# Kernel optimization log

Measured on AMD Instinct MI355X. Metric: run time of the kernel, lower is better.

## Reference

```python
import jax, jax.numpy as jnp
import numpy as np

D_MODEL = 1024
B, T = 4, 2048
NEG = -1000000000.0


def setup_inputs() -> dict:
    key = jax.random.key(0)
    kq, kk, kv = jax.random.split(key, 3)
    query = jax.random.normal(kq, (B, T, D_MODEL), dtype=jnp.float32)
    k = jax.random.normal(kk, (B, T, D_MODEL), dtype=jnp.float32)
    value = jax.random.normal(kv, (B, T, D_MODEL), dtype=jnp.float32)
    # causal mask: 1.0 where attention is disallowed (strictly upper triangular)
    mask = jnp.triu(jnp.ones((T, T), dtype=jnp.float32), k=1)
    return {"query": query, "key": k, "value": value, "mask": mask}


def reference(query, key, value, mask):
    # dk = sqrt(1/d_model); logits = QK^T / dk  (i.e. * sqrt(d_model)) -- faithful to source
    dk = jnp.sqrt(jnp.float32(1.0) / jnp.float32(D_MODEL))
    attn_logits = jnp.einsum("btc,bsc->bts", query, key) / dk
    attn_logits = attn_logits + mask * NEG  # mask broadcasts over batch
    score = jax.nn.softmax(attn_logits, axis=-1)
    attention = jnp.einsum("bts,bsc->btc", score, value)
    return attention
```

## Files before the change

### kernel.cpp

```cpp
#include <hip/hip_runtime.h>

#define BB 4
#define TT 2048
#define DD 1024
#define SCALE 32.0f
#define NTILE 136

typedef _Float16 f16;
typedef __attribute__((ext_vector_type(4))) _Float16 half4v;
typedef __attribute__((ext_vector_type(8))) _Float16 half8v;
typedef __attribute__((ext_vector_type(16))) float f32x16;

static __device__ inline half8v ld_frag(const f16* p) {
    half4v a = *(const half4v*)p;
    half4v b = *(const half4v*)(p + 4);
    half8v r;
    r[0] = a[0]; r[1] = a[1]; r[2] = a[2]; r[3] = a[3];
    r[4] = b[0]; r[5] = b[1]; r[6] = b[2]; r[7] = b[3];
    return r;
}

__global__ __launch_bounds__(256, 2) void k1_qk(const float* __restrict__ Q,
                                                const float* __restrict__ Kmat,
                                                float* __restrict__ S) {
    __shared__ f16 Ah[128][36], Al[128][36], Bh[128][36], Bl[128][36];

    int bid = blockIdx.x;
    int b = bid / NTILE, r = bid % NTILE;
    int mi = 0;
    while ((mi + 1) * (mi + 2) / 2 <= r) ++mi;
    int nj = r - mi * (mi + 1) / 2;

    const float* Qb = Q + ((size_t)b * TT + (size_t)mi * 128) * DD;
    const float* Kb = Kmat + ((size_t)b * TT + (size_t)nj * 128) * DD;
    float* Sb = S + (size_t)b * TT * TT + (size_t)(mi * 128) * TT + nj * 128;

    int tid = threadIdx.x;
    int lane = tid & 63;
    int wave = tid >> 6;
    int l31 = lane & 31, lhi = lane >> 5;
    int wrow = wave >> 1, wcol = wave & 1;

    int r0 = tid >> 1;
    int c0 = (tid & 1) * 16;

    f32x16 acc[2][2] = {};

    float4 abuf[4], bbuf[4];
#pragma unroll
    for (int j = 0; j < 4; ++j) {
        abuf[j] = *(const float4*)(Qb + (size_t)r0 * DD + c0 + 4 * j);
        bbuf[j] = *(const float4*)(Kb + (size_t)r0 * DD + c0 + 4 * j);
    }

    for (int ch = 0; ch < DD / 32; ++ch) {
        __syncthreads();
#pragma unroll
        for (int j = 0; j < 4; ++j) {
            float4 a = abuf[j], bq = bbuf[j];
            float ax[4] = {a.x * SCALE, a.y * SCALE, a.z * SCALE, a.w * SCALE};
            float bx[4] = {bq.x, bq.y, bq.z, bq.w};
            half4v ahv, alv, bhv, blv;
#pragma unroll
            for (int e = 0; e < 4; ++e) {
                f16 h = (f16)ax[e];
                ahv[e] = h;
                alv[e] = (f16)(ax[e] - (float)h);
                f16 g = (f16)bx[e];
                bhv[e] = g;
                blv[e] = (f16)(bx[e] - (float)g);
            }
            *(half4v*)&Ah[r0][c0 + 4 * j] = ahv;
            *(half4v*)&Al[r0][c0 + 4 * j] = alv;
            *(half4v*)&Bh[r0][c0 + 4 * j] = bhv;
            *(half4v*)&Bl[r0][c0 + 4 * j] = blv;
        }
        __syncthreads();
        if (ch + 1 < DD / 32) {
            int ck = (ch + 1) * 32;
#pragma unroll
            for (int j = 0; j < 4; ++j) {
                abuf[j] = *(const float4*)(Qb + (size_t)r0 * DD + ck + c0 + 4 * j);
                bbuf[j] = *(const float4*)(Kb + (size_t)r0 * DD + ck + c0 + 4 * j);
            }
        }
#pragma unroll
        for (int ks = 0; ks < 2; ++ks) {
            int kb = ks * 16 + lhi * 8;
            half8v ahf[2], alf[2], bhf[2], blf[2];
#pragma unroll
            for (int f = 0; f < 2; ++f) {
                ahf[f] = ld_frag(&Ah[wrow * 64 + f * 32 + l31][kb]);
                alf[f] = ld_frag(&Al[wrow * 64 + f * 32 + l31][kb]);
                bhf[f] = ld_frag(&Bh[wcol * 64 + f * 32 + l31][kb]);
                blf[f] = ld_frag(&Bl[wcol * 64 + f * 32 + l31][kb]);
            }
#pragma unroll
            for (int fm = 0; fm < 2; ++fm)
#pragma unroll
                for (int fn = 0; fn < 2; ++fn) {
                    acc[fm][fn] = __builtin_amdgcn_mfma_f32_32x32x16_f16(ahf[fm], bhf[fn], acc[fm][fn], 0, 0, 0);
                    acc[fm][fn] = __builtin_amdgcn_mfma_f32_32x32x16_f16(ahf[fm], blf[fn], acc[fm][fn], 0, 0, 0);
                    acc[fm][fn] = __builtin_amdgcn_mfma_f32_32x32x16_f16(alf[fm], bhf[fn], acc[fm][fn], 0, 0, 0);
                }
        }
    }
#pragma unroll
    for (int fm = 0; fm < 2; ++fm)
#pragma unroll
        for (int fn = 0; fn < 2; ++fn)
#pragma unroll
            for (int g = 0; g < 16; ++g) {
                int rr = (g & 3) + 8 * (g >> 2) + 4 * lhi;
                int row = wrow * 64 + fm * 32 + rr;
                int col = wcol * 64 + fn * 32 + l31;
                Sb[(size_t)row * TT + col] = acc[fm][fn][g];
            }
}

__global__ __launch_bounds__(256) void k1b_softmax(const float* __restrict__ S,
                                                   f16* __restrict__ P) {
    __shared__ float red[4];
    int rowid = blockIdx.x;
    int b = rowid >> 11, t = rowid & (TT - 1);
    const float* Sr = S + (size_t)b * TT * TT + (size_t)t * TT;
    f16* Pr = P + (size_t)b * TT * TT + (size_t)t * TT;
    int tid = threadIdx.x;
    int nv = t + 1;
    int rowend = ((t >> 7) + 1) << 7;

    float m = -3.0e38f;
    for (int c = tid; c < nv; c += 256) m = fmaxf(m, Sr[c]);
#pragma unroll
    for (int o = 32; o > 0; o >>= 1) m = fmaxf(m, __shfl_xor(m, o));
    if ((tid & 63) == 0) red[tid >> 6] = m;
    __syncthreads();
    m = fmaxf(fmaxf(red[0], red[1]), fmaxf(red[2], red[3]));
    __syncthreads();

    float s = 0.f;
    for (int c = tid; c < nv; c += 256) s += exp2f((Sr[c] - m) * 1.4426950408889634f);
#pragma unroll
    for (int o = 32; o > 0; o >>= 1) s += __shfl_xor(s, o);
    if ((tid & 63) == 0) red[tid >> 6] = s;
    __syncthreads();
    s = red[0] + red[1] + red[2] + red[3];
    float inv = 1.0f / s;

    for (int c = tid; c < rowend; c += 256) {
        float p = (c < nv) ? exp2f((Sr[c] - m) * 1.4426950408889634f) * inv : 0.0f;
        Pr[c] = (f16)p;
    }
}

__global__ __launch_bounds__(256, 2) void k2_pv(const f16* __restrict__ P,
                                                const float* __restrict__ V,
                                                float* __restrict__ O) {
    __shared__ f16 Pa[128][36];
    __shared__ f16 Vt[128][36];

    int bid = blockIdx.x;
    int b = bid >> 7;
    int rest = bid & 127;
    int mi = rest >> 3, nj = rest & 7;
    int kend = (mi + 1) * 128;

    const f16* Pb = P + (size_t)b * TT * TT + (size_t)(mi * 128) * TT;
    const float* Vb = V + (size_t)b * TT * DD + nj * 128;
    float* Ob = O + (size_t)b * TT * DD + (size_t)(mi * 128) * DD + nj * 128;

    int tid = threadIdx.x;
    int lane = tid & 63;
    int wave = tid >> 6;
    int l31 = lane & 31, lhi = lane >> 5;
    int wrow = wave >> 1, wcol = wave & 1;

    f32x16 acc[2][2] = {};

    int pr = tid >> 1, pc = (tid & 1) * 16;
    int vk = tid >> 3, vn = (tid & 7) * 16;

    uint2 pbuf[4];
    float4 vbuf[4];
#pragma unroll
    for (int j = 0; j < 4; ++j) {
        pbuf[j] = *(const uint2*)(Pb + (size_t)pr * TT + pc + 4 * j);
        vbuf[j] = *(const float4*)(Vb + (size_t)vk * DD + vn + 4 * j);
    }

    for (int ck = 0; ck < kend; ck += 32) {
        __syncthreads();
#pragma unroll
        for (int j = 0; j < 4; ++j) {
            *(uint2*)&Pa[pr][pc + 4 * j] = pbuf[j];
            float4 v = vbuf[j];
            float vv[4] = {v.x, v.y, v.z, v.w};
            int n0 = vn + 4 * j;
#pragma unroll
            for (int e = 0; e < 4; ++e) {
                int n = n0 + e;
                Vt[n][vk ^ ((((unsigned)n >> 4) & 3) << 3)] = (f16)vv[e];
            }
        }
        __syncthreads();
        if (ck + 32 < kend) {
            int cn = ck + 32;
#pragma unroll
            for (int j = 0; j < 4; ++j) {
                pbuf[j] = *(const uint2*)(Pb + (size_t)pr * TT + cn + pc + 4 * j);
                vbuf[j] = *(const float4*)(Vb + (size_t)(cn + vk) * DD + vn + 4 * j);
            }
        }
#pragma unroll
        for (int ks = 0; ks < 2; ++ks) {
            int kb = ks * 16 + lhi * 8;
            half8v paf[2], vbf[2];
#pragma unroll
            for (int f = 0; f < 2; ++f) {
                paf[f] = ld_frag(&Pa[wrow * 64 + f * 32 + l31][kb]);
                int n = wcol * 64 + f * 32 + l31;
                int kbs = kb ^ ((((unsigned)n >> 4) & 3) << 3);
                vbf[f] = ld_frag(&Vt[n][kbs]);
            }
#pragma unroll
            for (int fm = 0; fm < 2; ++fm)
#pragma unroll
                for (int fn = 0; fn < 2; ++fn)
                    acc[fm][fn] = __builtin_amdgcn_mfma_f32_32x32x16_f16(paf[fm], vbf[fn], acc[fm][fn], 0, 0, 0);
        }
    }
#pragma unroll
    for (int fm = 0; fm < 2; ++fm)
#pragma unroll
        for (int fn = 0; fn < 2; ++fn)
#pragma unroll
            for (int g = 0; g < 16; ++g) {
                int rr = (g & 3) + 8 * (g >> 2) + 4 * lhi;
                int row = wrow * 64 + fm * 32 + rr;
                int col = wcol * 64 + fn * 32 + l31;
                Ob[(size_t)row * DD + col] = acc[fm][fn][g];
            }
}

__global__ __launch_bounds__(256) void fa_fallback(const float* __restrict__ Q,
                                                   const float* __restrict__ Kmat,
                                                   const float* __restrict__ V,
                                                   float* __restrict__ O) {
    __shared__ float qs[DD];
    __shared__ float osum[DD];
    __shared__ float red[4];
    int rowid = blockIdx.x;
    int b = rowid >> 11, t = rowid & (TT - 1);
    const float* q = Q + ((size_t)b * TT + t) * DD;
    int tid = threadIdx.x;
    for (int j = tid; j < DD; j += 256) { qs[j] = q[j] * SCALE; osum[j] = 0.f; }
    __syncthreads();
    float m = -3.0e38f, l = 0.f;
    for (int s = 0; s <= t; ++s) {
        const float* kr = Kmat + ((size_t)b * TT + s) * DD;
        float part = 0.f;
#pragma unroll
        for (int j = 0; j < 4; ++j) part += qs[tid * 4 + j] * kr[tid * 4 + j];
#pragma unroll
        for (int o = 32; o > 0; o >>= 1) part += __shfl_xor(part, o);
        if ((tid & 63) == 0) red[tid >> 6] = part;
        __syncthreads();
        float dot = red[0] + red[1] + red[2] + red[3];
        float mn = fmaxf(m, dot);
        float f = exp2f((m - mn) * 1.44269504f);
        float e = exp2f((dot - mn) * 1.44269504f);
        l = l * f + e;
        const float* vr = V + ((size_t)b * TT + s) * DD;
#pragma unroll
        for (int j = 0; j < 4; ++j) {
            int c = tid * 4 + j;
            osum[c] = osum[c] * f + e * vr[c];
        }
        m = mn;
        __syncthreads();
    }
    float inv = 1.f / l;
    for (int j = tid; j < DD; j += 256) O[((size_t)b * TT + t) * DD + j] = osum[j] * inv;
}

extern "C" void kernel_launch(void* const* d_in, const int* in_sizes, int n_in,
                              void* d_out, int out_size, void* d_ws, size_t ws_size,
                              hipStream_t stream) {
    const float* Q = (const float*)d_in[0];
    const float* K = (const float*)d_in[1];
    const float* V = (const float*)d_in[2];
    float* O = (float*)d_out;

    size_t sbytes = (size_t)BB * TT * TT * 4;
    size_t pbytes = (size_t)BB * TT * TT * 2;

    if (ws_size >= sbytes + pbytes) {
        float* S = (float*)d_ws;
        f16* P = (f16*)((char*)d_ws + sbytes);
        hipLaunchKernelGGL(k1_qk, dim3(BB * NTILE), dim3(256), 0, stream, Q, K, S);
        hipLaunchKernelGGL(k1b_softmax, dim3(BB * TT), dim3(256), 0, stream, S, P);
        hipLaunchKernelGGL(k2_pv, dim3(BB * 16 * 8), dim3(256), 0, stream, P, V, O);
    } else {
        hipLaunchKernelGGL(fa_fallback, dim3(BB * TT), dim3(256), 0, stream, Q, K, V, O);
    }
}
```

Measured before the change: 181.0 us.

## Pre-pack Q/K/V to swizzled fp16 tiles and stream them via direct global-to-LDS loads

Adds pre-pass kernels that convert Q and K into split hi/lo fp16 tiles and transpose V into swizzled fp16 tiles. The QK and PV GEMMs then load these tiles straight into LDS with double-buffered global_load_lds, instead of converting through registers inside the main loop. Softmax now writes P directly in the tiled layout, and block IDs are remapped to improve cache locality. This adds extra passes and workspace traffic, and P reuses the Qt region of the workspace.

```diff
diff --git a/kernel.cpp b/kernel.cpp
--- a/kernel.cpp
+++ b/kernel.cpp
@@ -5,11 +5,19 @@
 #define DD 1024
 #define SCALE 32.0f
 #define NTILE 136
+#define L2E 1.4426950408889634f
 
 typedef _Float16 f16;
 typedef __attribute__((ext_vector_type(4))) _Float16 half4v;
 typedef __attribute__((ext_vector_type(8))) _Float16 half8v;
 typedef __attribute__((ext_vector_type(16))) float f32x16;
+
+typedef const __attribute__((address_space(1))) unsigned int* gas_u32;
+typedef __attribute__((address_space(3))) unsigned int* las_u32;
+
+static __device__ inline void gload16(const void* g, void* l) {
+    __builtin_amdgcn_global_load_lds((gas_u32)g, (las_u32)l, 16, 0, 0);
+}
 
 static __device__ inline half8v ld_frag(const f16* p) {
     half4v a = *(const half4v*)p;
@@ -20,39 +28,320 @@
     return r;
 }
 
+
+__global__ __launch_bounds__(256) void repack_qk(const float* __restrict__ Q,
+                                                 const float* __restrict__ K,
+                                                 f16* __restrict__ Qt,
+                                                 f16* __restrict__ Kt) {
+    const int total = 2 * BB * TT * (DD / 8);
+    for (int gid = blockIdx.x * 256 + threadIdx.x; gid < total; gid += gridDim.x * 256) {
+        int g = gid & 127;
+        int t = (gid >> 7) & 2047;
+        int b = (gid >> 18) & 3;
+        int which = gid >> 20;
+        const float* src = which ? K : Q;
+        f16* dst = which ? Kt : Qt;
+        float sc = which ? 1.0f : SCALE;
+        const float* p = src + ((size_t)(b * TT + t)) * DD + g * 8;
+        float4 x0 = *(const float4*)p;
+        float4 x1 = *(const float4*)(p + 4);
+        float vv[8] = {x0.x, x0.y, x0.z, x0.w, x1.x, x1.y, x1.z, x1.w};
+        half8v hi, lo;
+#pragma unroll
+        for (int e = 0; e < 8; ++e) {
+            float x = vv[e] * sc;
+            f16 h = (f16)x;
+            hi[e] = h;
+            lo[e] = (f16)(x - (float)h);
+        }
+        int r = t & 127, mi = t >> 7, ck = g >> 2, gq = g & 3;
+        char* base = (char*)dst + ((size_t)((b * 16 + mi) * 32 + ck)) * 16384 + r * 128;
+        *(half8v*)(base + ((gq ^ (r & 7)) << 4)) = hi;
+        *(half8v*)(base + (((4 + gq) ^ (r & 7)) << 4)) = lo;
+    }
+}
+
+__global__ __launch_bounds__(256) void transpose_v(const float* __restrict__ V,
+                                                   f16* __restrict__ Vt) {
+    __shared__ float Vs[64][129];
+    int bid = blockIdx.x;
+    int b = bid >> 8, kb = (bid >> 3) & 31, nj = bid & 7;
+    const float* src = V + ((size_t)(b * TT + kb * 64)) * DD + nj * 128;
+    int tid = threadIdx.x;
+#pragma unroll
+    for (int it = 0; it < 8; ++it) {
+        int f4 = it * 256 + tid;
+        int row = f4 >> 5, c4 = f4 & 31;
+        float4 x = *(const float4*)(src + (size_t)row * DD + c4 * 4);
+        Vs[row][c4 * 4 + 0] = x.x;
+        Vs[row][c4 * 4 + 1] = x.y;
+        Vs[row][c4 * 4 + 2] = x.z;
+        Vs[row][c4 * 4 + 3] = x.w;
+    }
+    __syncthreads();
+    char* dbase = (char*)Vt + ((size_t)((b * 8 + nj) * 32 + kb)) * 16384;
+#pragma unroll
+    for (int it = 0; it < 4; ++it) {
+        int gid = it * 256 + tid;
+        int n = gid >> 3, s = gid & 7;
+        half8v h;
+#pragma unroll
+        for (int j = 0; j < 8; ++j) h[j] = (f16)Vs[s * 8 + j][n];
+        *(half8v*)(dbase + n * 128 + ((s ^ (n & 7)) << 4)) = h;
+    }
+}
+
+__global__ __launch_bounds__(256, 2) void k1_qk2(const f16* __restrict__ Qt,
+                                                 const f16* __restrict__ Kt,
+                                                 float* __restrict__ S) {
+    __shared__ char lds[65536];
+
+    int bid0 = blockIdx.x;
+    int bid = (bid0 & 7) * (BB * NTILE / 8) + (bid0 >> 3);
+    int b = bid / NTILE, r = bid % NTILE;
+    int mi = 0;
+    while ((mi + 1) * (mi + 2) / 2 <= r) ++mi;
+    int nj = r - mi * (mi + 1) / 2;
+
+    const char* Abase = (const char*)Qt + ((size_t)((b * 16 + mi) * 32)) * 16384;
+    const char* Bbase = (const char*)Kt + ((size_t)((b * 16 + nj) * 32)) * 16384;
+    float* Sb = S + (size_t)b * TT * TT + (size_t)(mi * 128) * TT + nj * 128;
+
+    int tid = threadIdx.x;
+    int lane = tid & 63;
+    int wv = tid >> 6;
+    int l31 = lane & 31, lhi = lane >> 5;
+    int wrow = wv >> 1, wcol = wv & 1;
+
+    int aoff[2][2], boff[2][2];
+#pragma unroll
+    for (int fm = 0; fm < 2; ++fm) {
+        int ra = wrow * 64 + fm * 32 + l31;
+        int rb = wcol * 64 + fm * 32 + l31;
+#pragma unroll
+        for (int ks = 0; ks < 2; ++ks) {
+            int slot = ks * 2 + lhi;
+            aoff[fm][ks] = ra * 128 + ((slot ^ (ra & 7)) << 4);
+            boff[fm][ks] = rb * 128 + ((slot ^ (rb & 7)) << 4);
+        }
+    }
+    int lane_go = (wv * 256 + lane) * 16;
+    int lane_lo = (wv * 256) * 16;
+
+    f32x16 acc[2][2] = {};
+
+#define K1_STAGE(CK, BUF)                                                       \
+    {                                                                           \
+        const char* ga = Abase + (size_t)(CK) * 16384 + lane_go;                \
+        const char* gb = Bbase + (size_t)(CK) * 16384 + lane_go;                \
+        char* la = lds + (BUF) * 32768 + lane_lo;                               \
+        char* lb = la + 16384;                                                  \
+        _Pragma("unroll") for (int i = 0; i < 4; ++i)                           \
+            gload16(ga + i * 1024, la + i * 1024);                              \
+        _Pragma("unroll") for (int i = 0; i < 4; ++i)                           \
+            gload16(gb + i * 1024, lb + i * 1024);                              \
+    }
+
+    K1_STAGE(0, 0);
+    int cur = 0;
+    for (int ck = 0; ck < 32; ++ck) {
+        __syncthreads();
+        if (ck + 1 < 32) K1_STAGE(ck + 1, cur ^ 1);
+        const char* As = lds + cur * 32768;
+        const char* Bs = As + 16384;
+#pragma unroll
+        for (int ks = 0; ks < 2; ++ks) {
+            half8v ah[2], al[2], bh[2], bl[2];
+#pragma unroll
+            for (int f = 0; f < 2; ++f) {
+                ah[f] = *(const half8v*)(As + aoff[f][ks]);
+                al[f] = *(const half8v*)(As + (aoff[f][ks] ^ 64));
+                bh[f] = *(const half8v*)(Bs + boff[f][ks]);
+                bl[f] = *(const half8v*)(Bs + (boff[f][ks] ^ 64));
+            }
+#pragma unroll
+            for (int fm = 0; fm < 2; ++fm)
+#pragma unroll
+                for (int fn = 0; fn < 2; ++fn) {
+                    acc[fm][fn] = __builtin_amdgcn_mfma_f32_32x32x16_f16(ah[fm], bh[fn], acc[fm][fn], 0, 0, 0);
+                    acc[fm][fn] = __builtin_amdgcn_mfma_f32_32x32x16_f16(ah[fm], bl[fn], acc[fm][fn], 0, 0, 0);
+                    acc[fm][fn] = __builtin_amdgcn_mfma_f32_32x32x16_f16(al[fm], bh[fn], acc[fm][fn], 0, 0, 0);
+                }
+        }
+        cur ^= 1;
+    }
+#pragma unroll
+    for (int fm = 0; fm < 2; ++fm)
+#pragma unroll
+        for (int fn = 0; fn < 2; ++fn)
+#pragma unroll
+            for (int g = 0; g < 16; ++g) {
+                int rr = (g & 3) + 8 * (g >> 2) + 4 * lhi;
+                int row = wrow * 64 + fm * 32 + rr;
+                int col = wcol * 64 + fn * 32 + l31;
+                Sb[(size_t)row * TT + col] = acc[fm][fn][g];
+            }
+}
+
+__global__ __launch_bounds__(256) void k1b2(const float* __restrict__ S,
+                                            f16* __restrict__ Pt) {
+    __shared__ float red[4];
+    int rowid = blockIdx.x;
+    int b = rowid >> 11, t = rowid & (TT - 1);
+    const float* Sr = S + ((size_t)b * TT + t) * TT;
+    int tid = threadIdx.x;
+    int nv = t + 1;
+    int mi = t >> 7, r = t & 127;
+    int rowend = (mi + 1) << 7;
+    int c = tid * 8;
+
+    float4 x0 = *(const float4*)(Sr + c);
+    float4 x1 = *(const float4*)(Sr + c + 4);
+    float v[8] = {x0.x, x0.y, x0.z, x0.w, x1.x, x1.y, x1.z, x1.w};
+
+    float m = -3.0e38f;
+#pragma unroll
+    for (int j = 0; j < 8; ++j)
+        if (c + j < nv) m = fmaxf(m, v[j]);
+#pragma unroll
+    for (int o = 32; o > 0; o >>= 1) m = fmaxf(m, __shfl_xor(m, o));
+    if ((tid & 63) == 0) red[tid >> 6] = m;
+    __syncthreads();
+    m = fmaxf(fmaxf(red[0], red[1]), fmaxf(red[2], red[3]));
+    __syncthreads();
+
+    float e[8];
+    float s = 0.f;
+#pragma unroll
+    for (int j = 0; j < 8; ++j) {
+        e[j] = (c + j < nv) ? exp2f((v[j] - m) * L2E) : 0.0f;
+        s += e[j];
+    }
+#pragma unroll
+    for (int o = 32; o > 0; o >>= 1) s += __shfl_xor(s, o);
+    if ((tid & 63) == 0) red[tid >> 6] = s;
+    __syncthreads();
+    s = red[0] + red[1] + red[2] + red[3];
+    float inv = 1.0f / s;
+
+    if (c < rowend) {
+        half8v h;
+#pragma unroll
+        for (int j = 0; j < 8; ++j) h[j] = (f16)(e[j] * inv);
+        char* dst = (char*)Pt + ((size_t)((b * 16 + mi) * 32 + (c >> 6))) * 16384
+                    + r * 128 + ((((c >> 3) & 7) ^ (r & 7)) << 4);
+        *(half8v*)dst = h;
+    }
+}
+
+__global__ __launch_bounds__(256, 2) void k2_pv2(const f16* __restrict__ Pt,
+                                                 const f16* __restrict__ Vt,
+                                                 float* __restrict__ O) {
+    __shared__ char lds[65536];
+
+    int bid0 = blockIdx.x;
+    int bid = (bid0 & 7) * (512 / 8) + (bid0 >> 3);
+    int b = bid >> 7, mi = (bid >> 3) & 15, nj = bid & 7;
+    int kc = (mi + 1) * 2;
+
+    const char* Abase = (const char*)Pt + ((size_t)((b * 16 + mi) * 32)) * 16384;
+    const char* Bbase = (const char*)Vt + ((size_t)((b * 8 + nj) * 32)) * 16384;
+    float* Ob = O + (size_t)b * TT * DD + (size_t)(mi * 128) * DD + nj * 128;
+
+    int tid = threadIdx.x;
+    int lane = tid & 63;
+    int wv = tid >> 6;
+    int l31 = lane & 31, lhi = lane >> 5;
+    int wrow = wv >> 1, wcol = wv & 1;
+
+    int aoff[2][4], boff[2][4];
+#pragma unroll
+    for (int f = 0; f < 2; ++f) {
+        int ra = wrow * 64 + f * 32 + l31;
+        int rb = wcol * 64 + f * 32 + l31;
+#pragma unroll
+        for (int ks = 0; ks < 4; ++ks) {
+            int slot = ks * 2 + lhi;
+            aoff[f][ks] = ra * 128 + ((slot ^ (ra & 7)) << 4);
+            boff[f][ks] = rb * 128 + ((slot ^ (rb & 7)) << 4);
+        }
+    }
+    int lane_go = (wv * 256 + lane) * 16;
+    int lane_lo = (wv * 256) * 16;
+
+    f32x16 acc[2][2] = {};
+
+#define K2_STAGE(CK, BUF)                                                       \
+    {                                                                           \
+        const char* ga = Abase + (size_t)(CK) * 16384 + lane_go;                \
+        const char* gb = Bbase + (size_t)(CK) * 16384 + lane_go;                \
+        char* la = lds + (BUF) * 32768 + lane_lo;                               \
+        char* lb = la + 16384;                                                  \
+        _Pragma("unroll") for (int i = 0; i < 4; ++i)                           \
+            gload16(ga + i * 1024, la + i * 1024);                              \
+        _Pragma("unroll") for (int i = 0; i < 4; ++i)                           \
+            gload16(gb + i * 1024, lb + i * 1024);                              \
+    }
+
+    K2_STAGE(0, 0);
+    int cur = 0;
+    for (int ck = 0; ck < kc; ++ck) {
+        __syncthreads();
+        if (ck + 1 < kc) K2_STAGE(ck + 1, cur ^ 1);
+        const char* As = lds + cur * 32768;
+        const char* Bs = As + 16384;
+#pragma unroll
+        for (int ks = 0; ks < 4; ++ks) {
+            half8v a0 = *(const half8v*)(As + aoff[0][ks]);
+            half8v a1 = *(const half8v*)(As + aoff[1][ks]);
+            half8v b0 = *(const half8v*)(Bs + boff[0][ks]);
+            half8v b1 = *(const half8v*)(Bs + boff[1][ks]);
+            acc[0][0] = __builtin_amdgcn_mfma_f32_32x32x16_f16(a0, b0, acc[0][0], 0, 0, 0);
+            acc[0][1] = __builtin_amdgcn_mfma_f32_32x32x16_f16(a0, b1, acc[0][1], 0, 0, 0);
+            acc[1][0] = __builtin_amdgcn_mfma_f32_32x32x16_f16(a1, b0, acc[1][0], 0, 0, 0);
+            acc[1][1] = __builtin_amdgcn_mfma_f32_32x32x16_f16(a1, b1, acc[1][1], 0, 0, 0);
+        }
+        cur ^= 1;
+    }
+#pragma unroll
+    for (int fm = 0; fm < 2; ++fm)
+#pragma unroll
+        for (int fn = 0; fn < 2; ++fn)
+#pragma unroll
+            for (int g = 0; g < 16; ++g) {
+                int rr = (g & 3) + 8 * (g >> 2) + 4 * lhi;
+                int row = wrow * 64 + fm * 32 + rr;
+                int col = wcol * 64 + fn * 32 + l31;
+                Ob[(size_t)row * DD + col] = acc[fm][fn][g];
+            }
+}
+
 __global__ __launch_bounds__(256, 2) void k1_qk(const float* __restrict__ Q,
                                                 const float* __restrict__ Kmat,
                                                 float* __restrict__ S) {
     __shared__ f16 Ah[128][36], Al[128][36], Bh[128][36], Bl[128][36];
-
     int bid = blockIdx.x;
     int b = bid / NTILE, r = bid % NTILE;
     int mi = 0;
     while ((mi + 1) * (mi + 2) / 2 <= r) ++mi;
     int nj = r - mi * (mi + 1) / 2;
-
     const float* Qb = Q + ((size_t)b * TT + (size_t)mi * 128) * DD;
     const float* Kb = Kmat + ((size_t)b * TT + (size_t)nj * 128) * DD;
     float* Sb = S + (size_t)b * TT * TT + (size_t)(mi * 128) * TT + nj * 128;
-
     int tid = threadIdx.x;
     int lane = tid & 63;
     int wave = tid >> 6;
     int l31 = lane & 31, lhi = lane >> 5;
     int wrow = wave >> 1, wcol = wave & 1;
-
     int r0 = tid >> 1;
     int c0 = (tid & 1) * 16;
-
     f32x16 acc[2][2] = {};
-
     float4 abuf[4], bbuf[4];
 #pragma unroll
     for (int j = 0; j < 4; ++j) {
         abuf[j] = *(const float4*)(Qb + (size_t)r0 * DD + c0 + 4 * j);
         bbuf[j] = *(const float4*)(Kb + (size_t)r0 * DD + c0 + 4 * j);
     }
-
     for (int ch = 0; ch < DD / 32; ++ch) {
         __syncthreads();
 #pragma unroll
@@ -128,7 +417,6 @@
     int tid = threadIdx.x;
     int nv = t + 1;
     int rowend = ((t >> 7) + 1) << 7;
-
     float m = -3.0e38f;
     for (int c = tid; c < nv; c += 256) m = fmaxf(m, Sr[c]);
 #pragma unroll
@@ -137,18 +425,16 @@
     __syncthreads();
     m = fmaxf(fmaxf(red[0], red[1]), fmaxf(red[2], red[3]));
     __syncthreads();
-
     float s = 0.f;
-    for (int c = tid; c < nv; c += 256) s += exp2f((Sr[c] - m) * 1.4426950408889634f);
+    for (int c = tid; c < nv; c += 256) s += exp2f((Sr[c] - m) * L2E);
 #pragma unroll
     for (int o = 32; o > 0; o >>= 1) s += __shfl_xor(s, o);
     if ((tid & 63) == 0) red[tid >> 6] = s;
     __syncthreads();
     s = red[0] + red[1] + red[2] + red[3];
     float inv = 1.0f / s;
-
     for (int c = tid; c < rowend; c += 256) {
-        float p = (c < nv) ? exp2f((Sr[c] - m) * 1.4426950408889634f) * inv : 0.0f;
+        float p = (c < nv) ? exp2f((Sr[c] - m) * L2E) * inv : 0.0f;
         Pr[c] = (f16)p;
     }
 }
@@ -158,28 +444,22 @@
                                                 float* __restrict__ O) {
     __shared__ f16 Pa[128][36];
     __shared__ f16 Vt[128][36];
-
     int bid = blockIdx.x;
     int b = bid >> 7;
     int rest = bid & 127;
     int mi = rest >> 3, nj = rest & 7;
     int kend = (mi + 1) * 128;
-
     const f16* Pb = P + (size_t)b * TT * TT + (size_t)(mi * 128) * TT;
     const float* Vb = V + (size_t)b * TT * DD + nj * 128;
     float* Ob = O + (size_t)b * TT * DD + (size_t)(mi * 128) * DD + nj * 128;
-
     int tid = threadIdx.x;
     int lane = tid & 63;
     int wave = tid >> 6;
     int l31 = lane & 31, lhi = lane >> 5;
     int wrow = wave >> 1, wcol = wave & 1;
-
     f32x16 acc[2][2] = {};
-
     int pr = tid >> 1, pc = (tid & 1) * 16;
     int vk = tid >> 3, vn = (tid & 7) * 16;
-
     uint2 pbuf[4];
     float4 vbuf[4];
 #pragma unroll
@@ -187,7 +467,6 @@
         pbuf[j] = *(const uint2*)(Pb + (size_t)pr * TT + pc + 4 * j);
         vbuf[j] = *(const float4*)(Vb + (size_t)vk * DD + vn + 4 * j);
     }
-
     for (int ck = 0; ck < kend; ck += 32) {
         __syncthreads();
 #pragma unroll
@@ -291,10 +570,25 @@
     const float* V = (const float*)d_in[2];
     float* O = (float*)d_out;
 
+    const size_t MB = 1024 * 1024;
+    const size_t QT_B = 32 * MB, KT_B = 32 * MB, VT_B = 16 * MB, S_B = 64 * MB;
+    const size_t FULL = QT_B + KT_B + VT_B + S_B;
+
     size_t sbytes = (size_t)BB * TT * TT * 4;
     size_t pbytes = (size_t)BB * TT * TT * 2;
 
-    if (ws_size >= sbytes + pbytes) {
+    if (ws_size >= FULL) {
+        f16* Qt = (f16*)d_ws;
+        f16* Kt = (f16*)((char*)d_ws + QT_B);
+        f16* Vt = (f16*)((char*)d_ws + QT_B + KT_B);
+        float* S = (float*)((char*)d_ws + QT_B + KT_B + VT_B);
+        f16* Pt = (f16*)d_ws;
+        hipLaunchKernelGGL(repack_qk, dim3(2048), dim3(256), 0, stream, Q, K, Qt, Kt);
+        hipLaunchKernelGGL(transpose_v, dim3(1024), dim3(256), 0, stream, V, Vt);
+        hipLaunchKernelGGL(k1_qk2, dim3(BB * NTILE), dim3(256), 0, stream, Qt, Kt, S);
+        hipLaunchKernelGGL(k1b2, dim3(BB * TT), dim3(256), 0, stream, S, Pt);
+        hipLaunchKernelGGL(k2_pv2, dim3(512), dim3(256), 0, stream, Pt, Vt, O);
+    } else if (ws_size >= sbytes + pbytes) {
         float* S = (float*)d_ws;
         f16* P = (f16*)((char*)d_ws + sbytes);
         hipLaunchKernelGGL(k1_qk, dim3(BB * NTILE), dim3(256), 0, stream, Q, K, S);
```

After: 153.7 us. -15.1%, faster.
